# Performance work log

Measured on AMD Instinct MI355X. Metric: run time of the kernel, lower is better.

The kernel has to match this reference:

```python
import jax, jax.numpy as jnp
from jax import lax
import numpy as np

NUM_CLASSES = 7
EDGE_LO, EDGE_HI = 2, 7  # edge_classes = [2,3,4,5,6]
FOCAL_W, DICE_W, BOUND_W, TOPO_W = 0.3, 0.3, 0.2, 0.2
GAMMA = 2.0


def _dwconv(x, k):
    # depthwise 'same' conv with identical spatial kernel per channel
    C = x.shape[1]
    kern = jnp.broadcast_to(k[None, None], (C, 1) + k.shape)
    return lax.conv_general_dilated(
        x, kern, (1, 1), 'SAME',
        dimension_numbers=('NCHW', 'OIHW', 'NCHW'),
        feature_group_count=C)


def setup_inputs() -> dict:
    key = jax.random.key(0)
    k1, k2 = jax.random.split(key)
    logits = jax.random.normal(k1, (8, NUM_CLASSES, 512, 512), dtype=jnp.float32)
    targets = jax.random.randint(k2, (8, 512, 512), 0, NUM_CLASSES, dtype=jnp.int32)
    class_weights = jnp.ones((NUM_CLASSES,), dtype=jnp.float32)
    return {"logits": logits, "targets": targets, "class_weights": class_weights}


def reference(logits, targets, class_weights):
    C = logits.shape[1]
    logp = jax.nn.log_softmax(logits, axis=1)          # [B,C,H,W]
    probs = jnp.exp(logp)
    onehot = (targets[:, None, :, :] == jnp.arange(C)[None, :, None, None]).astype(logits.dtype)

    # ---- Focal loss (weighted CE, pt from the *weighted* CE as in torch code) ----
    nll = -jnp.take_along_axis(logp, targets[:, None].astype(jnp.int32), axis=1)[:, 0]  # [B,H,W]
    ce = class_weights[targets] * nll
    pt = jnp.exp(-ce)
    loss_focal = jnp.mean((1.0 - pt) ** GAMMA * ce)

    # ---- Dice loss (per class, global sums) ----
    inter = jnp.sum(probs * onehot, axis=(0, 2, 3))    # [C]
    union = jnp.sum(probs, axis=(0, 2, 3)) + jnp.sum(onehot, axis=(0, 2, 3))
    loss_dice = jnp.mean(1.0 - (2.0 * inter + 1e-6) / (union + 1e-6))

    # ---- Boundary loss ----
    lap = jnp.array([[0., 1., 0.], [1., -4., 1.], [0., 1., 0.]], dtype=jnp.float32)
    boundary = (jnp.abs(_dwconv(onehot, lap)) > 0).astype(jnp.float32)
    region = _dwconv(boundary, jnp.ones((5, 5), jnp.float32))
    bweight = 1.0 + 4.0 * (region > 0).astype(jnp.float32)
    bce = -onehot * jnp.log(probs + 1e-7) - (1.0 - onehot) * jnp.log(1.0 - probs + 1e-7)
    # sum_c mean_{B,H,W}(bce*w)/C == mean over [B,C,H,W]
    loss_boundary = jnp.mean(bce * bweight)

    # ---- Topology loss (edge classes 2..6) ----
    avg = jnp.ones((3, 3), jnp.float32) / 9.0
    pc = _dwconv(probs[:, EDGE_LO:EDGE_HI], avg)
    tc = _dwconv(onehot[:, EDGE_LO:EDGE_HI], avg)
    diff = jnp.abs(pc - tc)
    mask = onehot[:, EDGE_LO:EDGE_HI]
    msum = jnp.sum(mask, axis=(0, 2, 3))               # [5]
    num = jnp.sum(diff * mask, axis=(0, 2, 3))
    per_cls = jnp.where(msum >= 1.0, num / jnp.maximum(msum, 1.0), 0.0)
    loss_topo = jnp.sum(per_cls) / float(EDGE_HI - EDGE_LO)

    return FOCAL_W * loss_focal + DICE_W * loss_dice + BOUND_W * loss_boundary + TOPO_W * loss_topo
```

## Files before the change

kernel.cpp:

```cpp
#include <hip/hip_runtime.h>
#include <hip/hip_fp16.h>

#define BB 8
#define CC 7
#define HH 512
#define WW 512
#define HW (HH*WW)
#define NBLK 2048


__device__ __forceinline__ void softmax7x4(float4 a[7]) {
#pragma unroll
    for (int c = 0; c < 7; c++) {
        a[c].x = __expf(a[c].x); a[c].y = __expf(a[c].y);
        a[c].z = __expf(a[c].z); a[c].w = __expf(a[c].w);
    }
    float4 se = a[0];
#pragma unroll
    for (int c = 1; c < 7; c++) { se.x += a[c].x; se.y += a[c].y; se.z += a[c].z; se.w += a[c].w; }
    float ix = 1.f/se.x, iy = 1.f/se.y, iz = 1.f/se.z, iw = 1.f/se.w;
#pragma unroll
    for (int c = 0; c < 7; c++) { a[c].x *= ix; a[c].y *= iy; a[c].z *= iz; a[c].w *= iw; }
}

__device__ __forceinline__ void write_planes(unsigned short* sp, const float4 a[7], int r, int cI) {
#pragma unroll
    for (int c = 2; c < 7; c++) {
        unsigned lo = (unsigned)__half_as_ushort(__float2half_rn(a[c].x))
                    | ((unsigned)__half_as_ushort(__float2half_rn(a[c].y)) << 16);
        unsigned hi = (unsigned)__half_as_ushort(__float2half_rn(a[c].z))
                    | ((unsigned)__half_as_ushort(__float2half_rn(a[c].w)) << 16);
        uint2 w2 = make_uint2(lo, hi);
        *(uint2*)&sp[(c - 2) * 1360 + r * 40 + cI * 4] = w2;
    }
}

__device__ __forceinline__ void pixel_body(const float pr[7], int t, unsigned rmv,
                                           const unsigned short* sp, const unsigned char* st,
                                           const float* sw, int cy, int cx,
                                           float& accF, float& accB,
                                           float* sumP, float* inter, float* cnt, float* num) {
    float p_t = pr[0];
#pragma unroll
    for (int c = 1; c < 7; c++) p_t = (t == c) ? pr[c] : p_t;
    float ce = sw[t] * (-__logf(p_t));
    float ptv = __expf(-ce);
    float om = 1.0f - ptv;
    accF += om * om * ce;

    float prodA = 1.0f, prodB = 1.0f;
#pragma unroll
    for (int c = 0; c < 7; c++) {
        float p = pr[c];
        bool is = (c == t);
        sumP[c] += p;
        if (is) { inter[c] += p; cnt[c] += 1.0f; }
        float arg = is ? (p + 1e-7f) : (1.0f - p + 1e-7f);
        prodA *= arg;
        prodB *= ((rmv >> c) & 1u) ? arg : 1.0f;
    }
    accB -= __logf(prodA) + 4.0f * __logf(prodB);

    if ((unsigned)(t - 2) < 5u) {
        const unsigned short* pl = sp + (t - 2) * 1360;
        int base = (cy + 1) * 40 + (cx + 4);
        int sb = (cy + 3) * 40 + (cx + 4);
        float s = 0.f;
#pragma unroll
        for (int dy = -1; dy <= 1; dy++) {
#pragma unroll
            for (int dx = -1; dx <= 1; dx++) {
                float pn = __half2float(__ushort_as_half(pl[base + dy * 40 + dx]));
                s += pn - ((st[sb + dy * 40 + dx] == t) ? 1.0f : 0.0f);
            }
        }
        float val = fabsf(s) * (1.0f / 9.0f);
#pragma unroll
        for (int q = 0; q < 5; q++) num[q] += (t == q + 2) ? val : 0.f;
    }
}

__global__ __launch_bounds__(256) void main_kernel(const float* __restrict__ logits,
                                                   const int* __restrict__ tgt,
                                                   const float* __restrict__ cw,
                                                   float* __restrict__ part) {
    __shared__ unsigned short sp[5 * 1360];
    __shared__ unsigned char st[40 * 38];
    __shared__ unsigned char bm[36 * 36];
    __shared__ unsigned char hm[36 * 32];
    __shared__ unsigned char rm[1024];
    __shared__ float sw[8];
    __shared__ float sred[112];

    const int tid = threadIdx.x;
    const int b = blockIdx.z;
    const int gx0 = blockIdx.x * 32, gy0 = blockIdx.y * 32;
    if (tid < 7) sw[tid] = cw[tid];

    const float* lg = logits + (size_t)b * CC * HW;
    const int* tg = tgt + (size_t)b * HW;

    int4 tv0, tv1; bool tvld0, tvld1;
    {
        int r = tid / 10, cI = tid - r * 10;
        int y = gy0 - 3 + r, xs = gx0 - 4 + cI * 4;
        tvld0 = ((unsigned)y < HH) && ((unsigned)xs < WW);
        size_t off = tvld0 ? ((size_t)y * WW + xs) : 0;
        tv0 = *(const int4*)(tg + off);
    }
    {
        int g = tid + 256; int gc = (g < 380) ? g : 0;
        int r = gc / 10, cI = gc - r * 10;
        int y = gy0 - 3 + r, xs = gx0 - 4 + cI * 4;
        tvld1 = (g < 380) && ((unsigned)y < HH) && ((unsigned)xs < WW);
        size_t off = tvld1 ? ((size_t)y * WW + xs) : 0;
        tv1 = *(const int4*)(tg + off);
    }
    const int rI = 1 + (tid >> 3), cII = 1 + (tid & 7);
    float4 aI[7];
    {
        const float* p0 = lg + (size_t)(gy0 - 1 + rI) * WW + (gx0 - 4 + cII * 4);
#pragma unroll
        for (int c = 0; c < 7; c++) aI[c] = *(const float4*)(p0 + (size_t)c * HW);
    }
    float4 aH[7]; bool hvld = false; int hr = 0, hc = 0;
    if (tid < 84) {
        if (tid < 10)      { hr = 0;  hc = tid; }
        else if (tid < 20) { hr = 33; hc = tid - 10; }
        else { int e = tid - 20; hr = 1 + (e >> 1); hc = (e & 1) ? 9 : 0; }
        int y = gy0 - 1 + hr, xs = gx0 - 4 + hc * 4;
        hvld = ((unsigned)y < HH) && ((unsigned)xs < WW);
        size_t off = hvld ? ((size_t)y * WW + xs) : 0;
        const float* p0 = lg + off;
#pragma unroll
        for (int c = 0; c < 7; c++) aH[c] = *(const float4*)(p0 + (size_t)c * HW);
    }

    {
        int r = tid / 10, cI = tid - r * 10;
        unsigned w = tvld0 ? ((unsigned)tv0.x | ((unsigned)tv0.y << 8) |
                              ((unsigned)tv0.z << 16) | ((unsigned)tv0.w << 24))
                           : 0xFFFFFFFFu;
        *(unsigned*)&st[r * 40 + cI * 4] = w;
    }
    if (tid + 256 < 380) {
        int g = tid + 256;
        int r = g / 10, cI = g - r * 10;
        unsigned w = tvld1 ? ((unsigned)tv1.x | ((unsigned)tv1.y << 8) |
                              ((unsigned)tv1.z << 16) | ((unsigned)tv1.w << 24))
                           : 0xFFFFFFFFu;
        *(unsigned*)&st[r * 40 + cI * 4] = w;
    }

    softmax7x4(aI);
    write_planes(sp, aI, rI, cII);
    if (tid < 84) {
        if (hvld) {
            softmax7x4(aH);
        } else {
#pragma unroll
            for (int c = 0; c < 7; c++) aH[c] = make_float4(0.f, 0.f, 0.f, 0.f);
        }
        write_planes(sp, aH, hr, hc);
    }
    __syncthreads();

    for (int p = tid; p < 1296; p += 256) {
        int by = p / 36, bx = p - by * 36;
        int y = gy0 - 2 + by, x = gx0 - 2 + bx;
        unsigned bits = 0;
        if ((unsigned)y < HH && (unsigned)x < WW) {
            int si = (by + 1) * 40 + (bx + 2);
            int t = st[si];
            unsigned orm = 0; int nfirst = -1, same = 1, ninb = 0;
            int n;
            n = st[si - 40]; if (n != 255) { orm |= 1u << n; if (nfirst < 0) nfirst = n; else same &= (n == nfirst); ninb++; }
            n = st[si + 40]; if (n != 255) { orm |= 1u << n; if (nfirst < 0) nfirst = n; else same &= (n == nfirst); ninb++; }
            n = st[si - 1];  if (n != 255) { orm |= 1u << n; if (nfirst < 0) nfirst = n; else same &= (n == nfirst); ninb++; }
            n = st[si + 1];  if (n != 255) { orm |= 1u << n; if (nfirst < 0) nfirst = n; else same &= (n == nfirst); ninb++; }
            unsigned andm = (ninb == 4 && same) ? (1u << nfirst) : 0u;
            unsigned cbit = 1u << t;
            bits = (orm & ~cbit) | (cbit & ~andm);
        }
        bm[p] = (unsigned char)bits;
    }
    __syncthreads();
    for (int p = tid; p < 1152; p += 256) {
        int hy = p >> 5, hx = p & 31;
        const unsigned char* r = &bm[hy * 36 + hx];
        hm[p] = (unsigned char)(r[0] | r[1] | r[2] | r[3] | r[4]);
    }
    __syncthreads();
#pragma unroll
    for (int k = 0; k < 4; k++) {
        int p = tid + k * 256;
        const unsigned char* hc2 = &hm[(p >> 5) * 32 + (p & 31)];
        rm[p] = (unsigned char)(hc2[0] | hc2[32] | hc2[64] | hc2[96] | hc2[128]);
    }
    __syncthreads();

    float accF = 0.f, accB = 0.f;
    float sumP[7] = {0,0,0,0,0,0,0};
    float inter[7] = {0,0,0,0,0,0,0};
    float cnt[7] = {0,0,0,0,0,0,0};
    float num[5] = {0,0,0,0,0};
    const int cy = tid >> 3, cxb = (tid & 7) * 4;
    unsigned rmv4 = *(unsigned*)&rm[cy * 32 + cxb];
    unsigned t4 = *(unsigned*)&st[(cy + 3) * 40 + cxb + 4];
    {
        float pr[7] = {aI[0].x, aI[1].x, aI[2].x, aI[3].x, aI[4].x, aI[5].x, aI[6].x};
        pixel_body(pr, (int)(t4 & 255u), rmv4 & 255u, sp, st, sw, cy, cxb + 0,
                   accF, accB, sumP, inter, cnt, num);
    }
    {
        float pr[7] = {aI[0].y, aI[1].y, aI[2].y, aI[3].y, aI[4].y, aI[5].y, aI[6].y};
        pixel_body(pr, (int)((t4 >> 8) & 255u), (rmv4 >> 8) & 255u, sp, st, sw, cy, cxb + 1,
                   accF, accB, sumP, inter, cnt, num);
    }
    {
        float pr[7] = {aI[0].z, aI[1].z, aI[2].z, aI[3].z, aI[4].z, aI[5].z, aI[6].z};
        pixel_body(pr, (int)((t4 >> 16) & 255u), (rmv4 >> 16) & 255u, sp, st, sw, cy, cxb + 2,
                   accF, accB, sumP, inter, cnt, num);
    }
    {
        float pr[7] = {aI[0].w, aI[1].w, aI[2].w, aI[3].w, aI[4].w, aI[5].w, aI[6].w};
        pixel_body(pr, (int)((t4 >> 24) & 255u), (rmv4 >> 24) & 255u, sp, st, sw, cy, cxb + 3,
                   accF, accB, sumP, inter, cnt, num);
    }

    float vals[28];
    vals[0] = accF; vals[1] = accB;
#pragma unroll
    for (int c = 0; c < 7; c++) { vals[2+c] = sumP[c]; vals[9+c] = inter[c]; vals[16+c] = cnt[c]; }
#pragma unroll
    for (int j = 0; j < 5; j++) vals[23+j] = num[j];

    int lane = tid & 63, wid = tid >> 6;
#pragma unroll
    for (int i = 0; i < 28; i++) {
        float v = vals[i];
#pragma unroll
        for (int o = 32; o > 0; o >>= 1) v += __shfl_down(v, o, 64);
        if (lane == 0) sred[wid * 28 + i] = v;
    }
    __syncthreads();
    if (tid < 28) {
        float s = sred[tid] + sred[28 + tid] + sred[56 + tid] + sred[84 + tid];
        int bid = (blockIdx.z * gridDim.y + blockIdx.y) * gridDim.x + blockIdx.x;
        part[tid * NBLK + bid] = s;
    }
}

__global__ __launch_bounds__(256) void reduce_kernel(const float* __restrict__ part,
                                                     float* __restrict__ out) {
    __shared__ double swred[4];
    __shared__ double fin[28];
    const int tid = threadIdx.x;
    for (int j = 0; j < 28; j++) {
        double s = 0.0;
#pragma unroll
        for (int k = 0; k < NBLK / 256; k++) s += (double)part[j * NBLK + tid + k * 256];
#pragma unroll
        for (int o = 32; o > 0; o >>= 1) s += __shfl_down(s, o, 64);
        if ((tid & 63) == 0) swred[tid >> 6] = s;
        __syncthreads();
        if (tid == 0) fin[j] = swred[0] + swred[1] + swred[2] + swred[3];
        __syncthreads();
    }
    if (tid == 0) {
        double focal = fin[0] / (double)((size_t)BB * HW);
        double bound = fin[1] / (double)((size_t)BB * CC * HW);
        double dice = 0.0;
#pragma unroll
        for (int c = 0; c < 7; c++) {
            double uni = fin[2 + c] + fin[16 + c];
            dice += 1.0 - (2.0 * fin[9 + c] + 1e-6) / (uni + 1e-6);
        }
        dice *= (1.0 / 7.0);
        double topo = 0.0;
#pragma unroll
        for (int j = 0; j < 5; j++) {
            double ms = fin[18 + j];
            double nm = fin[23 + j];
            topo += (ms >= 1.0) ? nm / fmax(ms, 1.0) : 0.0;
        }
        topo *= (1.0 / 5.0);
        out[0] = (float)(0.3 * focal + 0.3 * dice + 0.2 * bound + 0.2 * topo);
    }
}

extern "C" void kernel_launch(void* const* d_in, const int* in_sizes, int n_in,
                              void* d_out, int out_size, void* d_ws, size_t ws_size,
                              hipStream_t stream) {
    const float* logits = (const float*)d_in[0];
    const int* tgt = (const int*)d_in[1];
    const float* cw = (const float*)d_in[2];
    float* out = (float*)d_out;
    float* part = (float*)d_ws;

    dim3 grid(WW / 32, HH / 32, BB);
    main_kernel<<<grid, 256, 0, stream>>>(logits, tgt, cw, part);
    reduce_kernel<<<1, 256, 0, stream>>>(part, out);
}
```

Before: 160.5 us.

## Process two vertical tiles per block with prefetch and DPP reductions

Each block now handles two stacked 32x32 tiles. The second tile's targets and logits are loaded while the first tile's masks and loss terms are computed, so global latency overlaps with work. The grid is halved, which halves the partial count, and the reduce kernel uses 1024 threads with one wave per statistic instead of serialized block-wide loops. The wave reduction switches from shuffles to DPP row operations. Register pressure from holding the extra float4 arrays may reduce occupancy.

```diff
diff --git a/kernel.cpp b/kernel.cpp
--- a/kernel.cpp
+++ b/kernel.cpp
@@ -6,8 +6,16 @@
 #define HH 512
 #define WW 512
 #define HW (HH*WW)
-#define NBLK 2048
-
+#define NBLK 1024
+
+
+__device__ __forceinline__ float dpp_red(float v) {
+#define STEP(ctrl) v += __int_as_float(__builtin_amdgcn_update_dpp(0, __float_as_int(v), ctrl, 0xF, 0xF, true))
+    STEP(0x111); STEP(0x112); STEP(0x114); STEP(0x118);
+    STEP(0x142); STEP(0x143);
+#undef STEP
+    return v;
+}
 
 __device__ __forceinline__ void softmax7x4(float4 a[7]) {
 #pragma unroll
@@ -30,8 +38,7 @@
                     | ((unsigned)__half_as_ushort(__float2half_rn(a[c].y)) << 16);
         unsigned hi = (unsigned)__half_as_ushort(__float2half_rn(a[c].z))
                     | ((unsigned)__half_as_ushort(__float2half_rn(a[c].w)) << 16);
-        uint2 w2 = make_uint2(lo, hi);
-        *(uint2*)&sp[(c - 2) * 1360 + r * 40 + cI * 4] = w2;
+        *(uint2*)&sp[(c - 2) * 1360 + r * 40 + cI * 4] = make_uint2(lo, hi);
     }
 }
 
@@ -80,50 +87,54 @@
     }
 }
 
-__global__ __launch_bounds__(256) void main_kernel(const float* __restrict__ logits,
-                                                   const int* __restrict__ tgt,
-                                                   const float* __restrict__ cw,
-                                                   float* __restrict__ part) {
-    __shared__ unsigned short sp[5 * 1360];
-    __shared__ unsigned char st[40 * 38];
-    __shared__ unsigned char bm[36 * 36];
-    __shared__ unsigned char hm[36 * 32];
-    __shared__ unsigned char rm[1024];
-    __shared__ float sw[8];
-    __shared__ float sred[112];
-
-    const int tid = threadIdx.x;
-    const int b = blockIdx.z;
-    const int gx0 = blockIdx.x * 32, gy0 = blockIdx.y * 32;
-    if (tid < 7) sw[tid] = cw[tid];
-
-    const float* lg = logits + (size_t)b * CC * HW;
-    const int* tg = tgt + (size_t)b * HW;
-
-    int4 tv0, tv1; bool tvld0, tvld1;
+__device__ __forceinline__ void load_tgt(int tid, int gy0, int gx0, const int* tg,
+                                         int4& tv0, bool& v0, int4& tv1, bool& v1) {
     {
         int r = tid / 10, cI = tid - r * 10;
         int y = gy0 - 3 + r, xs = gx0 - 4 + cI * 4;
-        tvld0 = ((unsigned)y < HH) && ((unsigned)xs < WW);
-        size_t off = tvld0 ? ((size_t)y * WW + xs) : 0;
+        v0 = ((unsigned)y < HH) && ((unsigned)xs < WW);
+        size_t off = v0 ? ((size_t)y * WW + xs) : 0;
         tv0 = *(const int4*)(tg + off);
     }
     {
         int g = tid + 256; int gc = (g < 380) ? g : 0;
         int r = gc / 10, cI = gc - r * 10;
         int y = gy0 - 3 + r, xs = gx0 - 4 + cI * 4;
-        tvld1 = (g < 380) && ((unsigned)y < HH) && ((unsigned)xs < WW);
-        size_t off = tvld1 ? ((size_t)y * WW + xs) : 0;
+        v1 = (g < 380) && ((unsigned)y < HH) && ((unsigned)xs < WW);
+        size_t off = v1 ? ((size_t)y * WW + xs) : 0;
         tv1 = *(const int4*)(tg + off);
     }
+}
+
+__device__ __forceinline__ void store_st(int tid, int4 tv0, bool v0, int4 tv1, bool v1,
+                                         unsigned char* st) {
+    {
+        int r = tid / 10, cI = tid - r * 10;
+        unsigned w = v0 ? ((unsigned)tv0.x | ((unsigned)tv0.y << 8) |
+                           ((unsigned)tv0.z << 16) | ((unsigned)tv0.w << 24))
+                        : 0xFFFFFFFFu;
+        *(unsigned*)&st[r * 40 + cI * 4] = w;
+    }
+    if (tid + 256 < 380) {
+        int g = tid + 256;
+        int r = g / 10, cI = g - r * 10;
+        unsigned w = v1 ? ((unsigned)tv1.x | ((unsigned)tv1.y << 8) |
+                           ((unsigned)tv1.z << 16) | ((unsigned)tv1.w << 24))
+                        : 0xFFFFFFFFu;
+        *(unsigned*)&st[r * 40 + cI * 4] = w;
+    }
+}
+
+__device__ __forceinline__ void load_int(int tid, int gy0, int gx0, const float* lg, float4 aI[7]) {
     const int rI = 1 + (tid >> 3), cII = 1 + (tid & 7);
-    float4 aI[7];
-    {
-        const float* p0 = lg + (size_t)(gy0 - 1 + rI) * WW + (gx0 - 4 + cII * 4);
-#pragma unroll
-        for (int c = 0; c < 7; c++) aI[c] = *(const float4*)(p0 + (size_t)c * HW);
-    }
-    float4 aH[7]; bool hvld = false; int hr = 0, hc = 0;
+    const float* p0 = lg + (size_t)(gy0 - 1 + rI) * WW + (gx0 - 4 + cII * 4);
+#pragma unroll
+    for (int c = 0; c < 7; c++) aI[c] = *(const float4*)(p0 + (size_t)c * HW);
+}
+
+__device__ __forceinline__ void load_halo(int tid, int gy0, int gx0, const float* lg,
+                                          float4 aH[7], bool& hvld, int& hr, int& hc) {
+    hvld = false; hr = 0; hc = 0;
     if (tid < 84) {
         if (tid < 10)      { hr = 0;  hc = tid; }
         else if (tid < 20) { hr = 33; hc = tid - 10; }
@@ -135,25 +146,10 @@
 #pragma unroll
         for (int c = 0; c < 7; c++) aH[c] = *(const float4*)(p0 + (size_t)c * HW);
     }
-
-    {
-        int r = tid / 10, cI = tid - r * 10;
-        unsigned w = tvld0 ? ((unsigned)tv0.x | ((unsigned)tv0.y << 8) |
-                              ((unsigned)tv0.z << 16) | ((unsigned)tv0.w << 24))
-                           : 0xFFFFFFFFu;
-        *(unsigned*)&st[r * 40 + cI * 4] = w;
-    }
-    if (tid + 256 < 380) {
-        int g = tid + 256;
-        int r = g / 10, cI = g - r * 10;
-        unsigned w = tvld1 ? ((unsigned)tv1.x | ((unsigned)tv1.y << 8) |
-                              ((unsigned)tv1.z << 16) | ((unsigned)tv1.w << 24))
-                           : 0xFFFFFFFFu;
-        *(unsigned*)&st[r * 40 + cI * 4] = w;
-    }
-
-    softmax7x4(aI);
-    write_planes(sp, aI, rI, cII);
+}
+
+__device__ __forceinline__ void halo_softmax_store(int tid, float4 aH[7], bool hvld,
+                                                   int hr, int hc, unsigned short* sp) {
     if (tid < 84) {
         if (hvld) {
             softmax7x4(aH);
@@ -163,8 +159,11 @@
         }
         write_planes(sp, aH, hr, hc);
     }
-    __syncthreads();
-
+}
+
+__device__ __forceinline__ void build_masks(int tid, int gy0, int gx0,
+                                            const unsigned char* st, unsigned char* bm,
+                                            unsigned char* hm, unsigned char* rm) {
     for (int p = tid; p < 1296; p += 256) {
         int by = p / 36, bx = p - by * 36;
         int y = gy0 - 2 + by, x = gx0 - 2 + bx;
@@ -198,35 +197,103 @@
         rm[p] = (unsigned char)(hc2[0] | hc2[32] | hc2[64] | hc2[96] | hc2[128]);
     }
     __syncthreads();
+}
+
+__device__ __forceinline__ void phase_b(int tid, const float4 aI[7],
+                                        const unsigned short* sp, const unsigned char* st,
+                                        const unsigned char* rm, const float* sw,
+                                        float& accF, float& accB,
+                                        float* sumP, float* inter, float* cnt, float* num) {
+    const int cy = tid >> 3, cxb = (tid & 7) * 4;
+    unsigned rmv4 = *(const unsigned*)&rm[cy * 32 + cxb];
+    unsigned t4 = *(const unsigned*)&st[(cy + 3) * 40 + cxb + 4];
+    {
+        float pr[7] = {aI[0].x, aI[1].x, aI[2].x, aI[3].x, aI[4].x, aI[5].x, aI[6].x};
+        pixel_body(pr, (int)(t4 & 255u), rmv4 & 255u, sp, st, sw, cy, cxb + 0,
+                   accF, accB, sumP, inter, cnt, num);
+    }
+    {
+        float pr[7] = {aI[0].y, aI[1].y, aI[2].y, aI[3].y, aI[4].y, aI[5].y, aI[6].y};
+        pixel_body(pr, (int)((t4 >> 8) & 255u), (rmv4 >> 8) & 255u, sp, st, sw, cy, cxb + 1,
+                   accF, accB, sumP, inter, cnt, num);
+    }
+    {
+        float pr[7] = {aI[0].z, aI[1].z, aI[2].z, aI[3].z, aI[4].z, aI[5].z, aI[6].z};
+        pixel_body(pr, (int)((t4 >> 16) & 255u), (rmv4 >> 16) & 255u, sp, st, sw, cy, cxb + 2,
+                   accF, accB, sumP, inter, cnt, num);
+    }
+    {
+        float pr[7] = {aI[0].w, aI[1].w, aI[2].w, aI[3].w, aI[4].w, aI[5].w, aI[6].w};
+        pixel_body(pr, (int)((t4 >> 24) & 255u), (rmv4 >> 24) & 255u, sp, st, sw, cy, cxb + 3,
+                   accF, accB, sumP, inter, cnt, num);
+    }
+}
+
+__global__ __launch_bounds__(256) void main_kernel(const float* __restrict__ logits,
+                                                   const int* __restrict__ tgt,
+                                                   const float* __restrict__ cw,
+                                                   float* __restrict__ part) {
+    __shared__ unsigned short sp[5 * 1360];
+    __shared__ unsigned char st[40 * 38];
+    __shared__ unsigned char bm[36 * 36];
+    __shared__ unsigned char hm[36 * 32];
+    __shared__ unsigned char rm[1024];
+    __shared__ float sw[8];
+    __shared__ float sred[112];
+
+    const int tid = threadIdx.x;
+    const int b = blockIdx.z;
+    const int gx0 = blockIdx.x * 32;
+    const int gy0a = blockIdx.y * 64;
+    const int gy0b = blockIdx.y * 64 + 32;
+    if (tid < 7) sw[tid] = cw[tid];
+
+    const float* lg = logits + (size_t)b * CC * HW;
+    const int* tg = tgt + (size_t)b * HW;
 
     float accF = 0.f, accB = 0.f;
     float sumP[7] = {0,0,0,0,0,0,0};
     float inter[7] = {0,0,0,0,0,0,0};
     float cnt[7] = {0,0,0,0,0,0,0};
     float num[5] = {0,0,0,0,0};
-    const int cy = tid >> 3, cxb = (tid & 7) * 4;
-    unsigned rmv4 = *(unsigned*)&rm[cy * 32 + cxb];
-    unsigned t4 = *(unsigned*)&st[(cy + 3) * 40 + cxb + 4];
-    {
-        float pr[7] = {aI[0].x, aI[1].x, aI[2].x, aI[3].x, aI[4].x, aI[5].x, aI[6].x};
-        pixel_body(pr, (int)(t4 & 255u), rmv4 & 255u, sp, st, sw, cy, cxb + 0,
-                   accF, accB, sumP, inter, cnt, num);
-    }
-    {
-        float pr[7] = {aI[0].y, aI[1].y, aI[2].y, aI[3].y, aI[4].y, aI[5].y, aI[6].y};
-        pixel_body(pr, (int)((t4 >> 8) & 255u), (rmv4 >> 8) & 255u, sp, st, sw, cy, cxb + 1,
-                   accF, accB, sumP, inter, cnt, num);
-    }
-    {
-        float pr[7] = {aI[0].z, aI[1].z, aI[2].z, aI[3].z, aI[4].z, aI[5].z, aI[6].z};
-        pixel_body(pr, (int)((t4 >> 16) & 255u), (rmv4 >> 16) & 255u, sp, st, sw, cy, cxb + 2,
-                   accF, accB, sumP, inter, cnt, num);
-    }
-    {
-        float pr[7] = {aI[0].w, aI[1].w, aI[2].w, aI[3].w, aI[4].w, aI[5].w, aI[6].w};
-        pixel_body(pr, (int)((t4 >> 24) & 255u), (rmv4 >> 24) & 255u, sp, st, sw, cy, cxb + 3,
-                   accF, accB, sumP, inter, cnt, num);
-    }
+
+    int4 tv0, tv1; bool v0, v1;
+    load_tgt(tid, gy0a, gx0, tg, tv0, v0, tv1, v1);
+    float4 aI[7];
+    load_int(tid, gy0a, gx0, lg, aI);
+    float4 aH[7]; bool hvld; int hr, hc;
+    load_halo(tid, gy0a, gx0, lg, aH, hvld, hr, hc);
+
+    store_st(tid, tv0, v0, tv1, v1, st);
+    {
+        const int rI = 1 + (tid >> 3), cII = 1 + (tid & 7);
+        softmax7x4(aI);
+        write_planes(sp, aI, rI, cII);
+    }
+    halo_softmax_store(tid, aH, hvld, hr, hc, sp);
+
+    int4 u0, u1; bool w0, w1;
+    load_tgt(tid, gy0b, gx0, tg, u0, w0, u1, w1);
+    float4 aJ[7];
+    load_int(tid, gy0b, gx0, lg, aJ);
+
+    __syncthreads();
+    build_masks(tid, gy0a, gx0, st, bm, hm, rm);
+    phase_b(tid, aI, sp, st, rm, sw, accF, accB, sumP, inter, cnt, num);
+    __syncthreads();
+
+    store_st(tid, u0, w0, u1, w1, st);
+    {
+        const int rI = 1 + (tid >> 3), cII = 1 + (tid & 7);
+        softmax7x4(aJ);
+        write_planes(sp, aJ, rI, cII);
+    }
+    load_halo(tid, gy0b, gx0, lg, aH, hvld, hr, hc);
+    halo_softmax_store(tid, aH, hvld, hr, hc, sp);
+
+    __syncthreads();
+    build_masks(tid, gy0b, gx0, st, bm, hm, rm);
+    phase_b(tid, aJ, sp, st, rm, sw, accF, accB, sumP, inter, cnt, num);
 
     float vals[28];
     vals[0] = accF; vals[1] = accB;
@@ -235,13 +302,11 @@
 #pragma unroll
     for (int j = 0; j < 5; j++) vals[23+j] = num[j];
 
-    int lane = tid & 63, wid = tid >> 6;
+    const int lane = tid & 63, wid = tid >> 6;
 #pragma unroll
     for (int i = 0; i < 28; i++) {
-        float v = vals[i];
-#pragma unroll
-        for (int o = 32; o > 0; o >>= 1) v += __shfl_down(v, o, 64);
-        if (lane == 0) sred[wid * 28 + i] = v;
+        float v = dpp_red(vals[i]);
+        if (lane == 63) sred[wid * 28 + i] = v;
     }
     __syncthreads();
     if (tid < 28) {
@@ -251,22 +316,20 @@
     }
 }
 
-__global__ __launch_bounds__(256) void reduce_kernel(const float* __restrict__ part,
-                                                     float* __restrict__ out) {
-    __shared__ double swred[4];
+__global__ __launch_bounds__(1024) void reduce_kernel(const float* __restrict__ part,
+                                                      float* __restrict__ out) {
     __shared__ double fin[28];
     const int tid = threadIdx.x;
-    for (int j = 0; j < 28; j++) {
+    const int w = tid >> 6, lane = tid & 63;
+    for (int j = w; j < 28; j += 16) {
         double s = 0.0;
 #pragma unroll
-        for (int k = 0; k < NBLK / 256; k++) s += (double)part[j * NBLK + tid + k * 256];
+        for (int k = 0; k < NBLK / 64; k++) s += (double)part[j * NBLK + lane + k * 64];
 #pragma unroll
         for (int o = 32; o > 0; o >>= 1) s += __shfl_down(s, o, 64);
-        if ((tid & 63) == 0) swred[tid >> 6] = s;
-        __syncthreads();
-        if (tid == 0) fin[j] = swred[0] + swred[1] + swred[2] + swred[3];
-        __syncthreads();
-    }
+        if (lane == 0) fin[j] = s;
+    }
+    __syncthreads();
     if (tid == 0) {
         double focal = fin[0] / (double)((size_t)BB * HW);
         double bound = fin[1] / (double)((size_t)BB * CC * HW);
@@ -298,7 +361,7 @@
     float* out = (float*)d_out;
     float* part = (float*)d_ws;
 
-    dim3 grid(WW / 32, HH / 32, BB);
+    dim3 grid(WW / 32, HH / 64, BB);
     main_kernel<<<grid, 256, 0, stream>>>(logits, tgt, cw, part);
-    reduce_kernel<<<1, 256, 0, stream>>>(part, out);
-}
+    reduce_kernel<<<1, 1024, 0, stream>>>(part, out);
+}
```

Measured after the change: 135.8 us. 1.18x faster.
